# Performance work log

Hardware: AMD Instinct MI355X
Metric: run time of the kernel (lower is better)

## Reference

```python
import jax, jax.numpy as jnp
import numpy as np

# Config (matches init_kwargs)
L, K, N = 2048, 64, 8
CB, AB, G2 = 64, 8, 9
CSB, ASB, G3 = 16, 16, 3
ROUT_ITER = 3
B = 32
LN = L // N  # 256


def squash(s):
    sq = jnp.sum(s * s, axis=-1, keepdims=True)
    return sq / (1.0 + sq) * (s / jnp.sqrt(sq + 1e-8))


def conv1d(x, w, b, pad):
    # x: [B, Cin, L], w: [Cout, Cin, k]
    y = jax.lax.conv_general_dilated(x, w, window_strides=(1,), padding=[(pad, pad)],
                                     dimension_numbers=("NCH", "OIH", "NCH"))
    return y + b[None, :, None]


def routing(V, n_iters):
    # V: [B, Ln, n, cSB, aSB]
    b_logits = jnp.zeros(V.shape[:-1], dtype=V.dtype)
    v = None
    for r in range(n_iters):
        c = jax.nn.softmax(b_logits, axis=-1)[..., None]  # [B,Ln,n,cSB,1]
        s = jnp.sum(c * V, axis=-3)                        # [B,Ln,cSB,aSB]
        v = squash(s)
        if r < n_iters - 1:
            a = jnp.sum(V * v[..., None, :, :], axis=-1)   # [B,Ln,n,cSB]
            b_logits = b_logits + jax.lax.stop_gradient(a)
    return v


def setup_inputs() -> dict:
    key = jax.random.key(0)
    ks = jax.random.split(key, 7)
    x = jax.random.normal(ks[0], (B, K, L), dtype=jnp.float32)
    w0 = jax.random.normal(ks[1], (CB, K, 1), dtype=jnp.float32) * 0.05
    b0 = jnp.zeros((CB,), dtype=jnp.float32)
    w1 = jax.random.normal(ks[2], (CB * AB, CB, G2), dtype=jnp.float32) * 0.05
    b1 = jnp.zeros((CB * AB,), dtype=jnp.float32)
    w2 = jax.random.normal(ks[3], (CSB * ASB, 1, G3, CB * AB), dtype=jnp.float32) * 0.05
    b2 = jnp.zeros((CSB * ASB,), dtype=jnp.float32)
    return {"x": x, "w0": w0, "b0": b0, "w1": w1, "b1": b1, "w2": w2, "b2": b2}


def reference(x, w0, b0, w1, b1, w2, b2):
    # convLayer: 1x1 conv1d  [B,K,L] -> [B,CB,L]
    h = conv1d(x, w0, b0, pad=0)
    # conv1: 'same' padding, odd kernel G2 -> symmetric pad G2//2
    h = conv1d(h, w1, b1, pad=G2 // 2)  # [B, CB*AB, L]
    # -> [B, Ln, n, CB*AB], squash primary capsules
    h = jnp.transpose(h, (0, 2, 1)).reshape(B, LN, N, CB * AB)
    h = squash(h)
    # -> [B, 1, Ln, n*CB*AB]
    h = h.reshape(B, LN, N * CB * AB)[:, None, :, :]
    # conv2: kernel (G3, CB*AB), stride (1, CB*AB), pad (G3//2, 0)
    pad_h = int(G3 / 2 - 0.5)
    h = jax.lax.conv_general_dilated(h, w2, window_strides=(1, CB * AB),
                                     padding=[(pad_h, pad_h), (0, 0)],
                                     dimension_numbers=("NCHW", "OIHW", "NCHW"))
    h = h + b2[None, :, None, None]                  # [B, CSB*ASB, Ln, n]
    V = jnp.transpose(h, (0, 2, 3, 1)).reshape(B, LN, N, CSB, ASB)
    v = routing(V, ROUT_ITER)                        # [B, Ln, CSB, ASB]
    return v.reshape(B, LN * CSB, ASB)
```

## Files before the change

kernel.cpp:

```cpp
#include <hip/hip_runtime.h>


#define LL    2048
#define NCAP  8
#define CO1   512
#define CO2   256
#define LNN   256

typedef __attribute__((ext_vector_type(8))) short bhalf8;
typedef __attribute__((ext_vector_type(4))) float facc4;

#define MFMA16(a, b, c) __builtin_amdgcn_mfma_f32_16x16x32_bf16(a, b, c, 0, 0, 0)

__device__ inline unsigned short f2bf(float f) {
  unsigned u = __float_as_uint(f);
  return (unsigned short)((u + 0x7FFFu + ((u >> 16) & 1u)) >> 16);
}

#define OFF_W1TB 0u
#define OFF_W2B  589824u
#define OFF_H0T  1376256u
#define OFF_H1   9764864u
#define OFF_H1SQ 143982592u

__global__ __launch_bounds__(256) void prep_kernel(
    const float* __restrict__ w1, const float* __restrict__ w2,
    unsigned short* __restrict__ w1tb, unsigned short* __restrict__ w2b) {
  int idx = blockIdx.x * 256 + threadIdx.x;
  if (idx < 294912) {
    int cb = idx & 63;
    int co = (idx >> 6) & 511;
    int g  = idx >> 15;
    w1tb[idx] = f2bf(w1[(co * 64 + cb) * 9 + g]);
  } else {
    int j = idx - 294912;
    if (j < 393216) w2b[j] = f2bf(w2[j]);
  }
}

__global__ __launch_bounds__(256) void conv0_kernel(
    const float* __restrict__ x, const float* __restrict__ w0,
    const float* __restrict__ b0, unsigned short* __restrict__ h0t) {
  __shared__ __align__(16) float xt[64][128];
  __shared__ __align__(16) float w0t[64][68];
  int tid = threadIdx.x;
  int b = blockIdx.y;
  int l0 = blockIdx.x * 128;
  const float* xb = x + (size_t)b * 64 * LL;
#pragma unroll
  for (int i = 0; i < 8; i++) {
    int idx = i * 256 + tid;
    int k = idx >> 5, l4 = idx & 31;
    float4 v = *(const float4*)&xb[k * LL + l0 + l4 * 4];
    *(float4*)&xt[k][l4 * 4] = v;
  }
#pragma unroll
  for (int i = 0; i < 16; i++) {
    int idx = i * 256 + tid;
    int cb = idx >> 6, k = idx & 63;
    w0t[k][cb] = w0[idx];
  }
  __syncthreads();
  int lc = tid & 31, rc = tid >> 5;
  float acc[8][4] = {};
  for (int k = 0; k < 64; k++) {
    float4 bv = *(const float4*)&xt[k][lc * 4];
    float4 a0 = *(const float4*)&w0t[k][rc * 8];
    float4 a1 = *(const float4*)&w0t[k][rc * 8 + 4];
    float a[8] = {a0.x, a0.y, a0.z, a0.w, a1.x, a1.y, a1.z, a1.w};
    float bb4[4] = {bv.x, bv.y, bv.z, bv.w};
#pragma unroll
    for (int i = 0; i < 8; i++)
#pragma unroll
      for (int j = 0; j < 4; j++) acc[i][j] += a[i] * bb4[j];
  }
  float bias[8];
#pragma unroll
  for (int i = 0; i < 8; i++) bias[i] = b0[rc * 8 + i];
#pragma unroll
  for (int j = 0; j < 4; j++) {
    bhalf8 o;
#pragma unroll
    for (int i = 0; i < 8; i++) o[i] = (short)f2bf(acc[i][j] + bias[i]);
    *(bhalf8*)&h0t[((size_t)b * LL + l0 + lc * 4 + j) * 64 + rc * 8] = o;
  }
}

__global__ __launch_bounds__(512) void conv1_mfma(
    const unsigned short* __restrict__ h0t, const unsigned short* __restrict__ w1tb,
    const float* __restrict__ b1, float* __restrict__ h1) {
  __shared__ __align__(16) unsigned short Xt[136 * 72];
  __shared__ __align__(16) unsigned short Wg[256 * 72];
  int tid = threadIdx.x;
  int b = blockIdx.z;
  int co0 = blockIdx.y * 256;
  int l0 = blockIdx.x * 128;
#pragma unroll
  for (int it = 0; it < 3; it++) {
    int idx = it * 512 + tid;
    if (idx < 1088) {
      int row = idx >> 3, c8 = (idx & 7) * 8;
      int l = l0 - 4 + row;
      bhalf8 v = (bhalf8)0;
      if (l >= 0 && l < LL) v = *(const bhalf8*)&h0t[((size_t)b * LL + l) * 64 + c8];
      *(bhalf8*)&Xt[row * 72 + c8] = v;
    }
  }
  int wid = tid >> 6, lane = tid & 63;
  int wr = wid >> 1, wc = wid & 1;
  int r16 = lane & 15, k8 = lane >> 4;
  facc4 acc[4][4] = {};
  for (int g = 0; g < 9; g++) {
    __syncthreads();
#pragma unroll
    for (int it = 0; it < 4; it++) {
      int idx = it * 512 + tid;
      int row = idx >> 3, c8 = (idx & 7) * 8;
      *(bhalf8*)&Wg[row * 72 + c8] =
          *(const bhalf8*)&w1tb[((size_t)(g * 512 + co0 + row)) * 64 + c8];
    }
    __syncthreads();
#pragma unroll
    for (int ks = 0; ks < 2; ks++) {
      bhalf8 A[4], Bf[4];
#pragma unroll
      for (int mi = 0; mi < 4; mi++)
        A[mi] = *(const bhalf8*)&Wg[(wr * 64 + mi * 16 + r16) * 72 + ks * 32 + k8 * 8];
#pragma unroll
      for (int ni = 0; ni < 4; ni++)
        Bf[ni] = *(const bhalf8*)&Xt[(wc * 64 + ni * 16 + r16 + g) * 72 + ks * 32 + k8 * 8];
#pragma unroll
      for (int mi = 0; mi < 4; mi++)
#pragma unroll
        for (int ni = 0; ni < 4; ni++)
          acc[mi][ni] = MFMA16(A[mi], Bf[ni], acc[mi][ni]);
    }
  }
#pragma unroll
  for (int mi = 0; mi < 4; mi++) {
    int co_w = co0 + wr * 64 + mi * 16 + k8 * 4;
    float4 bias = *(const float4*)&b1[co_w];
#pragma unroll
    for (int ni = 0; ni < 4; ni++) {
      int l_w = l0 + wc * 64 + ni * 16 + r16;
      float* p = &h1[((size_t)b * LL + l_w) * CO1 + co_w];
      *(float4*)p = make_float4(acc[mi][ni][0] + bias.x, acc[mi][ni][1] + bias.y,
                                acc[mi][ni][2] + bias.z, acc[mi][ni][3] + bias.w);
    }
  }
}

__global__ __launch_bounds__(256) void squash1_kernel(
    const float* __restrict__ h1, unsigned short* __restrict__ h1sq) {
  int tid = threadIdx.x;
  int wave = tid >> 6, lane = tid & 63;
  size_t row = (size_t)blockIdx.x * 4 + wave;
  const float* p = h1 + row * CO1;
  float4 v0 = *(const float4*)(p + lane * 8);
  float4 v1 = *(const float4*)(p + lane * 8 + 4);
  float sq = v0.x * v0.x + v0.y * v0.y + v0.z * v0.z + v0.w * v0.w +
             v1.x * v1.x + v1.y * v1.y + v1.z * v1.z + v1.w * v1.w;
#pragma unroll
  for (int m = 1; m < 64; m <<= 1) sq += __shfl_xor(sq, m, 64);
  float s = sq / (1.f + sq) / sqrtf(sq + 1e-8f);
  bhalf8 o;
  o[0] = (short)f2bf(v0.x * s); o[1] = (short)f2bf(v0.y * s);
  o[2] = (short)f2bf(v0.z * s); o[3] = (short)f2bf(v0.w * s);
  o[4] = (short)f2bf(v1.x * s); o[5] = (short)f2bf(v1.y * s);
  o[6] = (short)f2bf(v1.z * s); o[7] = (short)f2bf(v1.w * s);
  *(bhalf8*)&h1sq[row * CO1 + lane * 8] = o;
}

__global__ __launch_bounds__(512) void conv2_mfma(
    const unsigned short* __restrict__ h1sq, const unsigned short* __restrict__ w2b,
    const float* __restrict__ b2, float* __restrict__ V) {
  __shared__ __align__(16) unsigned short Hc[130 * 72];
  __shared__ __align__(16) unsigned short Wgc[256 * 72];
  int tid = threadIdx.x;
  int bn = blockIdx.z;
  int b = bn >> 3, n = bn & 7;
  int ln0 = blockIdx.x * 128;
  int wid = tid >> 6, lane = tid & 63;
  int wr = wid >> 1, wc = wid & 1;
  int r16 = lane & 15, k8 = lane >> 4;
  facc4 acc[4][4] = {};
  for (int cc = 0; cc < 8; cc++) {
    int c0 = cc * 64;
    __syncthreads();
#pragma unroll
    for (int it = 0; it < 3; it++) {
      int idx = it * 512 + tid;
      if (idx < 1040) {
        int row = idx >> 3, c8 = (idx & 7) * 8;
        int ln = ln0 - 1 + row;
        bhalf8 v = (bhalf8)0;
        if (ln >= 0 && ln < LNN)
          v = *(const bhalf8*)&h1sq[((size_t)b * LL + ln * NCAP + n) * CO1 + c0 + c8];
        *(bhalf8*)&Hc[row * 72 + c8] = v;
      }
    }
    for (int g = 0; g < 3; g++) {
      __syncthreads();
#pragma unroll
      for (int it = 0; it < 4; it++) {
        int idx = it * 512 + tid;
        int row = idx >> 3, c8 = (idx & 7) * 8;
        *(bhalf8*)&Wgc[row * 72 + c8] =
            *(const bhalf8*)&w2b[((size_t)(row * 3 + g)) * CO1 + c0 + c8];
      }
      __syncthreads();
#pragma unroll
      for (int ks = 0; ks < 2; ks++) {
        bhalf8 A[4], Bf[4];
#pragma unroll
        for (int mi = 0; mi < 4; mi++)
          A[mi] = *(const bhalf8*)&Wgc[(wr * 64 + mi * 16 + r16) * 72 + ks * 32 + k8 * 8];
#pragma unroll
        for (int ni = 0; ni < 4; ni++)
          Bf[ni] = *(const bhalf8*)&Hc[(wc * 64 + ni * 16 + r16 + g) * 72 + ks * 32 + k8 * 8];
#pragma unroll
        for (int mi = 0; mi < 4; mi++)
#pragma unroll
          for (int ni = 0; ni < 4; ni++)
            acc[mi][ni] = MFMA16(A[mi], Bf[ni], acc[mi][ni]);
      }
    }
  }
#pragma unroll
  for (int mi = 0; mi < 4; mi++) {
    int o_w = wr * 64 + mi * 16 + k8 * 4;
    float4 bias = *(const float4*)&b2[o_w];
#pragma unroll
    for (int ni = 0; ni < 4; ni++) {
      int ln_w = ln0 + wc * 64 + ni * 16 + r16;
      float* p = &V[(((size_t)b * LNN + ln_w) * NCAP + n) * CO2 + o_w];
      *(float4*)p = make_float4(acc[mi][ni][0] + bias.x, acc[mi][ni][1] + bias.y,
                                acc[mi][ni][2] + bias.z, acc[mi][ni][3] + bias.w);
    }
  }
}

__global__ __launch_bounds__(256) void routing_kernel(
    const float* __restrict__ V, float* __restrict__ out) {
  __shared__ float Vs[8][16][17];
  __shared__ float blog[8][16];
  __shared__ float cbuf[8][16];
  __shared__ float vbuf[16][17];
  int tid = threadIdx.x;
  size_t base = (size_t)blockIdx.x * 2048;
#pragma unroll
  for (int i = 0; i < 8; i++) {
    int idx = i * 256 + tid;
    int nn = idx >> 8, r = idx & 255;
    Vs[nn][r >> 4][r & 15] = V[base + idx];
  }
  if (tid < 128) blog[tid >> 4][tid & 15] = 0.f;
  __syncthreads();
  int csb = tid >> 4, asb = tid & 15;
  for (int r = 0; r < 3; r++) {
    if (tid < 128) {
      int nn = tid >> 4, cs = tid & 15;
      float xv = blog[nn][cs];
      float m = xv;
#pragma unroll
      for (int d = 1; d < 16; d <<= 1) m = fmaxf(m, __shfl_xor(m, d, 16));
      float e = expf(xv - m);
      float ssum = e;
#pragma unroll
      for (int d = 1; d < 16; d <<= 1) ssum += __shfl_xor(ssum, d, 16);
      cbuf[nn][cs] = e / ssum;
    }
    __syncthreads();
    float s = 0.f;
#pragma unroll
    for (int q = 0; q < 8; q++) s += cbuf[q][csb] * Vs[q][csb][asb];
    float sq = s * s;
#pragma unroll
    for (int d = 1; d < 16; d <<= 1) sq += __shfl_xor(sq, d, 16);
    float vv = s * (sq / (1.f + sq) / sqrtf(sq + 1e-8f));
    if (r < 2) {
      vbuf[csb][asb] = vv;
      __syncthreads();
      if (tid < 128) {
        int nn = tid >> 4, cs = tid & 15;
        float a = 0.f;
#pragma unroll
        for (int q = 0; q < 16; q++) a += Vs[nn][cs][q] * vbuf[cs][q];
        blog[nn][cs] += a;
      }
      __syncthreads();
    } else {
      out[(size_t)blockIdx.x * 256 + tid] = vv;
    }
  }
}

extern "C" void kernel_launch(void* const* d_in, const int* in_sizes, int n_in,
                              void* d_out, int out_size, void* d_ws, size_t ws_size,
                              hipStream_t stream) {
  const float* x  = (const float*)d_in[0];
  const float* w0 = (const float*)d_in[1];
  const float* b0 = (const float*)d_in[2];
  const float* w1 = (const float*)d_in[3];
  const float* b1 = (const float*)d_in[4];
  const float* w2 = (const float*)d_in[5];
  const float* b2 = (const float*)d_in[6];
  float* out = (float*)d_out;
  char* ws = (char*)d_ws;
  unsigned short* w1tb = (unsigned short*)(ws + OFF_W1TB);
  unsigned short* w2b  = (unsigned short*)(ws + OFF_W2B);
  unsigned short* h0t  = (unsigned short*)(ws + OFF_H0T);
  float*          h1   = (float*)(ws + OFF_H1);
  unsigned short* h1sq = (unsigned short*)(ws + OFF_H1SQ);
  float*          Vb   = (float*)(ws + OFF_H1);

  prep_kernel<<<2688, 256, 0, stream>>>(w1, w2, w1tb, w2b);
  conv0_kernel<<<dim3(16, 32), 256, 0, stream>>>(x, w0, b0, h0t);
  conv1_mfma<<<dim3(16, 2, 32), 512, 0, stream>>>(h0t, w1tb, b1, h1);
  squash1_kernel<<<16384, 256, 0, stream>>>(h1, h1sq);
  conv2_mfma<<<dim3(2, 1, 256), 512, 0, stream>>>(h1sq, w2b, b2, Vb);
  routing_kernel<<<8192, 256, 0, stream>>>(Vb, out);
}
```

Before: 254.2 us.

## Restructure conv2 with pre-padded LDS layouts, direct global-to-LDS loads, larger tiles

The primary-capsule squash output and the conv2 weights are now written in a padded (72-stride), chunk-contiguous layout, so conv2 can copy whole chunks into LDS with global_load_lds. This falls back to vector copies when that builtin is unavailable. Each conv2 block now covers all 256 positions for one (b,n), and all three kernel taps' weights are loaded once per channel chunk. That cuts the number of barriers and removes the redundant halo and weight reloads. The cost is about 150KB of LDS per block and 128 accumulator registers per thread, so occupancy is lower and only 256 blocks are launched.

```diff
diff --git a/kernel.cpp b/kernel.cpp
--- a/kernel.cpp
+++ b/kernel.cpp
@@ -17,15 +17,32 @@
   return (unsigned short)((u + 0x7FFFu + ((u >> 16) & 1u)) >> 16);
 }
 
+#if __has_builtin(__builtin_amdgcn_global_load_lds)
+#define HAVE_GLDS 1
+#else
+#define HAVE_GLDS 0
+#endif
+
+__device__ __forceinline__ void g2l16(const unsigned short* g, unsigned short* l,
+                                      int lane) {
+#if HAVE_GLDS
+  __builtin_amdgcn_global_load_lds(
+      (const __attribute__((address_space(1))) void*)(g + lane * 8),
+      (__attribute__((address_space(3))) void*)l, 16, 0, 0);
+#else
+  *(bhalf8*)(l + lane * 8) = *(const bhalf8*)(g + lane * 8);
+#endif
+}
+
 #define OFF_W1TB 0u
-#define OFF_W2B  589824u
-#define OFF_H0T  1376256u
-#define OFF_H1   9764864u
-#define OFF_H1SQ 143982592u
+#define OFF_W2P  589824u
+#define OFF_H0T  1474560u
+#define OFF_H1   9863168u
+#define OFF_H1SQ 144080896u
 
 __global__ __launch_bounds__(256) void prep_kernel(
     const float* __restrict__ w1, const float* __restrict__ w2,
-    unsigned short* __restrict__ w1tb, unsigned short* __restrict__ w2b) {
+    unsigned short* __restrict__ w1tb, unsigned short* __restrict__ w2p) {
   int idx = blockIdx.x * 256 + threadIdx.x;
   if (idx < 294912) {
     int cb = idx & 63;
@@ -34,7 +51,14 @@
     w1tb[idx] = f2bf(w1[(co * 64 + cb) * 9 + g]);
   } else {
     int j = idx - 294912;
-    if (j < 393216) w2b[j] = f2bf(w2[j]);
+    int ci = j & 63;
+    int t  = j >> 6;
+    int o  = t & 255;
+    t >>= 8;
+    int g  = t % 3;
+    int cc = t / 3;
+    w2p[((cc * 3 + g) * 256 + o) * 72 + ci] =
+        f2bf(w2[(o * 3 + g) * 512 + cc * 64 + ci]);
   }
 }
 
@@ -168,71 +192,58 @@
   o[2] = (short)f2bf(v0.z * s); o[3] = (short)f2bf(v0.w * s);
   o[4] = (short)f2bf(v1.x * s); o[5] = (short)f2bf(v1.y * s);
   o[6] = (short)f2bf(v1.z * s); o[7] = (short)f2bf(v1.w * s);
-  *(bhalf8*)&h1sq[row * CO1 + lane * 8] = o;
-}
-
-__global__ __launch_bounds__(512) void conv2_mfma(
-    const unsigned short* __restrict__ h1sq, const unsigned short* __restrict__ w2b,
+  int b = (int)(row >> 11), l = (int)(row & 2047);
+  int ln = l >> 3, n = l & 7;
+  int cc = lane >> 3, ci8 = (lane & 7) * 8;
+  *(bhalf8*)&h1sq[((size_t)(((b * 8 + n) * 8 + cc) * 256 + ln)) * 72 + ci8] = o;
+}
+
+__global__ __launch_bounds__(512, 2) void conv2_mfma(
+    const unsigned short* __restrict__ h1sq, const unsigned short* __restrict__ w2p,
     const float* __restrict__ b2, float* __restrict__ V) {
-  __shared__ __align__(16) unsigned short Hc[130 * 72];
-  __shared__ __align__(16) unsigned short Wgc[256 * 72];
-  int tid = threadIdx.x;
-  int bn = blockIdx.z;
+  __shared__ __align__(16) unsigned short Hc[258 * 72];
+  __shared__ __align__(16) unsigned short Wl[3 * 256 * 72];
+  int tid = threadIdx.x;
+  int bn = blockIdx.x;
   int b = bn >> 3, n = bn & 7;
-  int ln0 = blockIdx.x * 128;
   int wid = tid >> 6, lane = tid & 63;
-  int wr = wid >> 1, wc = wid & 1;
+  int wr = wid >> 2, wc = wid & 3;
   int r16 = lane & 15, k8 = lane >> 4;
-  facc4 acc[4][4] = {};
+  facc4 acc[8][4] = {};
   for (int cc = 0; cc < 8; cc++) {
-    int c0 = cc * 64;
-    __syncthreads();
-#pragma unroll
-    for (int it = 0; it < 3; it++) {
-      int idx = it * 512 + tid;
-      if (idx < 1040) {
-        int row = idx >> 3, c8 = (idx & 7) * 8;
-        int ln = ln0 - 1 + row;
-        bhalf8 v = (bhalf8)0;
-        if (ln >= 0 && ln < LNN)
-          v = *(const bhalf8*)&h1sq[((size_t)b * LL + ln * NCAP + n) * CO1 + c0 + c8];
-        *(bhalf8*)&Hc[row * 72 + c8] = v;
+    __syncthreads();
+    if (tid < 72) { Hc[tid] = 0; Hc[257 * 72 + tid] = 0; }
+    const unsigned short* hsrc = h1sq + (size_t)((b * 8 + n) * 8 + cc) * (256 * 72);
+    for (int ch = wid; ch < 36; ch += 8)
+      g2l16(hsrc + ch * 512, &Hc[72 + ch * 512], lane);
+    const unsigned short* wsrc = w2p + (size_t)cc * (3 * 256 * 72);
+    for (int ch = wid; ch < 108; ch += 8)
+      g2l16(wsrc + ch * 512, &Wl[ch * 512], lane);
+    __syncthreads();
+    for (int g = 0; g < 3; g++) {
+#pragma unroll
+      for (int ks = 0; ks < 2; ks++) {
+        bhalf8 Bv[4];
+#pragma unroll
+        for (int ni = 0; ni < 4; ni++)
+          Bv[ni] = *(const bhalf8*)&Hc[(wc * 64 + ni * 16 + r16 + g) * 72 + ks * 32 + k8 * 8];
+#pragma unroll
+        for (int mi = 0; mi < 8; mi++) {
+          bhalf8 Av = *(const bhalf8*)&Wl[(g * 256 + wr * 128 + mi * 16 + r16) * 72 + ks * 32 + k8 * 8];
+#pragma unroll
+          for (int ni = 0; ni < 4; ni++)
+            acc[mi][ni] = MFMA16(Av, Bv[ni], acc[mi][ni]);
+        }
       }
     }
-    for (int g = 0; g < 3; g++) {
-      __syncthreads();
-#pragma unroll
-      for (int it = 0; it < 4; it++) {
-        int idx = it * 512 + tid;
-        int row = idx >> 3, c8 = (idx & 7) * 8;
-        *(bhalf8*)&Wgc[row * 72 + c8] =
-            *(const bhalf8*)&w2b[((size_t)(row * 3 + g)) * CO1 + c0 + c8];
-      }
-      __syncthreads();
-#pragma unroll
-      for (int ks = 0; ks < 2; ks++) {
-        bhalf8 A[4], Bf[4];
-#pragma unroll
-        for (int mi = 0; mi < 4; mi++)
-          A[mi] = *(const bhalf8*)&Wgc[(wr * 64 + mi * 16 + r16) * 72 + ks * 32 + k8 * 8];
-#pragma unroll
-        for (int ni = 0; ni < 4; ni++)
-          Bf[ni] = *(const bhalf8*)&Hc[(wc * 64 + ni * 16 + r16 + g) * 72 + ks * 32 + k8 * 8];
-#pragma unroll
-        for (int mi = 0; mi < 4; mi++)
-#pragma unroll
-          for (int ni = 0; ni < 4; ni++)
-            acc[mi][ni] = MFMA16(A[mi], Bf[ni], acc[mi][ni]);
-      }
-    }
-  }
-#pragma unroll
-  for (int mi = 0; mi < 4; mi++) {
-    int o_w = wr * 64 + mi * 16 + k8 * 4;
+  }
+#pragma unroll
+  for (int mi = 0; mi < 8; mi++) {
+    int o_w = wr * 128 + mi * 16 + k8 * 4;
     float4 bias = *(const float4*)&b2[o_w];
 #pragma unroll
     for (int ni = 0; ni < 4; ni++) {
-      int ln_w = ln0 + wc * 64 + ni * 16 + r16;
+      int ln_w = wc * 64 + ni * 16 + r16;
       float* p = &V[(((size_t)b * LNN + ln_w) * NCAP + n) * CO2 + o_w];
       *(float4*)p = make_float4(acc[mi][ni][0] + bias.x, acc[mi][ni][1] + bias.y,
                                 acc[mi][ni][2] + bias.z, acc[mi][ni][3] + bias.w);
@@ -308,16 +319,16 @@
   float* out = (float*)d_out;
   char* ws = (char*)d_ws;
   unsigned short* w1tb = (unsigned short*)(ws + OFF_W1TB);
-  unsigned short* w2b  = (unsigned short*)(ws + OFF_W2B);
+  unsigned short* w2p  = (unsigned short*)(ws + OFF_W2P);
   unsigned short* h0t  = (unsigned short*)(ws + OFF_H0T);
   float*          h1   = (float*)(ws + OFF_H1);
   unsigned short* h1sq = (unsigned short*)(ws + OFF_H1SQ);
   float*          Vb   = (float*)(ws + OFF_H1);
 
-  prep_kernel<<<2688, 256, 0, stream>>>(w1, w2, w1tb, w2b);
+  prep_kernel<<<2688, 256, 0, stream>>>(w1, w2, w1tb, w2p);
   conv0_kernel<<<dim3(16, 32), 256, 0, stream>>>(x, w0, b0, h0t);
   conv1_mfma<<<dim3(16, 2, 32), 512, 0, stream>>>(h0t, w1tb, b1, h1);
   squash1_kernel<<<16384, 256, 0, stream>>>(h1, h1sq);
-  conv2_mfma<<<dim3(2, 1, 256), 512, 0, stream>>>(h1sq, w2b, b2, Vb);
+  conv2_mfma<<<256, 512, 0, stream>>>(h1sq, w2p, b2, Vb);
   routing_kernel<<<8192, 256, 0, stream>>>(Vb, out);
 }
```

Result: slower. 263.9 us (+3.8%).
